# Kernel optimization log

Measured on AMD Instinct MI355X. Metric: run time of the kernel, lower is better.

The kernel has to match this reference:

```python
import jax, jax.numpy as jnp
import numpy as np

N = 100000
E = 1600000
IN_FEATS = 128
H_FEATS = 128
NUM_CLASSES = 64
BN_EPS = 1e-5


def setup_inputs() -> dict:
    key = jax.random.key(0)
    ks = jax.random.split(key, 16)
    inp = {
        "in_feat": jax.random.normal(ks[0], (N, IN_FEATS), dtype=jnp.float32),
        "src": jax.random.randint(ks[1], (E,), 0, N, dtype=jnp.int64),
        "dst": jax.random.randint(ks[2], (E,), 0, N, dtype=jnp.int64),
        # GraphConv weights (glorot-ish scale) and biases
        "W0": jax.random.normal(ks[3], (IN_FEATS, H_FEATS), dtype=jnp.float32) / np.sqrt(IN_FEATS),
        "b0": jnp.zeros((H_FEATS,), dtype=jnp.float32),
        "W1": jax.random.normal(ks[4], (H_FEATS, H_FEATS), dtype=jnp.float32) / np.sqrt(H_FEATS),
        "b1": jnp.zeros((H_FEATS,), dtype=jnp.float32),
        "W2": jax.random.normal(ks[5], (H_FEATS, NUM_CLASSES), dtype=jnp.float32) / np.sqrt(H_FEATS),
        "b2": jnp.zeros((NUM_CLASSES,), dtype=jnp.float32),
        # BatchNorm affine params
        "gamma0": jnp.ones((H_FEATS,), dtype=jnp.float32),
        "beta0": jnp.zeros((H_FEATS,), dtype=jnp.float32),
        "gamma1": jnp.ones((H_FEATS,), dtype=jnp.float32),
        "beta1": jnp.zeros((H_FEATS,), dtype=jnp.float32),
    }
    return inp


def _graph_conv(src, dst, h, W, b):
    # DGL GraphConv, norm='both': D_dst^{-1/2} A (D_src^{-1/2} h W) + b
    ones = jnp.ones((src.shape[0],), dtype=h.dtype)
    deg_out = jnp.clip(jax.ops.segment_sum(ones, src, num_segments=N), 1.0)
    deg_in = jnp.clip(jax.ops.segment_sum(ones, dst, num_segments=N), 1.0)
    h = h * jax.lax.rsqrt(deg_out)[:, None]
    h = h @ W  # mult weight before aggregation (same math either way)
    agg = jax.ops.segment_sum(h[src], dst, num_segments=N)  # SpMM
    return agg * jax.lax.rsqrt(deg_in)[:, None] + b


def _batch_norm(h, gamma, beta):
    # BatchNorm1d in training mode: biased batch stats over the node axis
    mean = jnp.mean(h, axis=0)
    var = jnp.mean(jnp.square(h - mean), axis=0)
    return (h - mean) * jax.lax.rsqrt(var + BN_EPS) * gamma + beta


def reference(in_feat, src, dst, W0, b0, W1, b1, W2, b2, gamma0, beta0, gamma1, beta1):
    h = _graph_conv(src, dst, in_feat, W0, b0)
    h = jax.nn.relu(_batch_norm(h, gamma0, beta0))  # dropout p=0 -> identity
    h = _graph_conv(src, dst, h, W1, b1)
    h = jax.nn.relu(_batch_norm(h, gamma1, beta1))
    return _graph_conv(src, dst, h, W2, b2)
```

## Files before the change

kernel.cpp:

```cpp
#include <hip/hip_runtime.h>

#define NFEAT 128
#define BT 2048
#define BSH 9
#define BSZ 512

static inline size_t align_up(size_t x, size_t a) { return (x + a - 1) & ~(a - 1); }

__device__ inline unsigned short f2bf(float f) {
  unsigned u = __float_as_uint(f);
  u += 0x7FFF + ((u >> 16) & 1);
  return (unsigned short)(u >> 16);
}

__global__ __launch_bounds__(256) void k_bcount(const int* __restrict__ src,
                                                const int* __restrict__ dst,
                                                int* __restrict__ cnt, int E, int nb, int NBK) {
  __shared__ int hD[256], hS[256];
  const int t = threadIdx.x, b = blockIdx.x;
  hD[t] = 0; hS[t] = 0;
  __syncthreads();
  const int e0 = b * BT, e1 = min(E, e0 + BT);
  for (int e = e0 + t; e < e1; e += 256) {
    atomicAdd(&hD[dst[e] >> BSH], 1);
    atomicAdd(&hS[src[e] >> BSH], 1);
  }
  __syncthreads();
  if (t < NBK) {
    cnt[t * nb + b] = hD[t];
    cnt[(NBK + t) * nb + b] = hS[t];
  }
}

__global__ __launch_bounds__(512) void k_scanA(const int* __restrict__ in,
                                               int* __restrict__ out,
                                               int* __restrict__ bsum, int n) {
  __shared__ int tmp[512];
  const int t = threadIdx.x;
  const int i = blockIdx.x * 512 + t;
  int v = (i < n) ? in[i] : 0;
  tmp[t] = v;
  __syncthreads();
  for (int off = 1; off < 512; off <<= 1) {
    int y = (t >= off) ? tmp[t - off] : 0;
    __syncthreads();
    tmp[t] += y;
    __syncthreads();
  }
  int incl = tmp[t];
  if (i < n) out[i] = incl - v;
  if (t == 511) bsum[blockIdx.x] = incl;
}

__global__ __launch_bounds__(1024) void k_scanB(const int* __restrict__ bsum,
                                                int* __restrict__ bscan, int nb1) {
  __shared__ int tmp[1024];
  const int t = threadIdx.x;
  int v = (t < nb1) ? bsum[t] : 0;
  tmp[t] = v;
  __syncthreads();
  for (int off = 1; off < 1024; off <<= 1) {
    int y = (t >= off) ? tmp[t - off] : 0;
    __syncthreads();
    tmp[t] += y;
    __syncthreads();
  }
  bscan[t] = tmp[t] - v;
}

__global__ __launch_bounds__(512) void k_scanC(int* __restrict__ out,
                                               const int* __restrict__ bscan, int n) {
  const int i = blockIdx.x * 512 + threadIdx.x;
  if (i < n) out[i] += bscan[blockIdx.x];
}

__global__ __launch_bounds__(256) void k_bplace(const int* __restrict__ src,
                                                const int* __restrict__ dst,
                                                const int* __restrict__ off,
                                                int* __restrict__ buf, int E, int nb, int NBK) {
  __shared__ int cD[256], cS[256];
  const int t = threadIdx.x, b = blockIdx.x;
  if (t < NBK) {
    cD[t] = off[t * nb + b];
    cS[t] = off[(NBK + t) * nb + b];
  }
  __syncthreads();
  const int e0 = b * BT, e1 = min(E, e0 + BT);
  for (int e = e0 + t; e < e1; e += 256) {
    int s = src[e];
    int d = dst[e];
    int pD = atomicAdd(&cD[d >> BSH], 1);
    buf[pD] = ((d & (BSZ - 1)) << 17) | s;
    int pS = atomicAdd(&cS[s >> BSH], 1);
    buf[pS] = s;
  }
}

__global__ __launch_bounds__(256) void k_bcsr(const int* __restrict__ buf,
                                              const int* __restrict__ off,
                                              int* __restrict__ row_ptr,
                                              float* __restrict__ rsq_in,
                                              int* __restrict__ col,
                                              int E, int nb, int NBK, int N) {
  const int k = blockIdx.x, t = threadIdx.x;
  const int lo = off[k * nb];
  const int hi = (k + 1 < NBK) ? off[(k + 1) * nb] : E;
  __shared__ int cnt[BSZ];
  __shared__ int sc[BSZ];
  __shared__ int part[64];
  cnt[t] = 0; cnt[t + 256] = 0;
  __syncthreads();
  for (int e = lo + t; e < hi; e += 256) atomicAdd(&cnt[((unsigned)buf[e]) >> 17], 1);
  __syncthreads();
  if (t < 64) {
    int r = 0;
#pragma unroll
    for (int j = 0; j < 8; ++j) r += cnt[t * 8 + j];
    part[t] = r;
  }
  __syncthreads();
  if (t == 0) {
    int run = 0;
    for (int i = 0; i < 64; ++i) { int v = part[i]; part[i] = run; run += v; }
  }
  __syncthreads();
  if (t < 64) {
    int run = part[t];
#pragma unroll
    for (int j = 0; j < 8; ++j) { int v = cnt[t * 8 + j]; sc[t * 8 + j] = run; run += v; }
  }
  __syncthreads();
  for (int idx = t; idx < BSZ; idx += 256) {
    int n = (k << BSH) + idx;
    if (n < N) {
      row_ptr[n] = lo + sc[idx];
      int c = cnt[idx]; if (c < 1) c = 1;
      rsq_in[n] = 1.0f / sqrtf((float)c);
    }
    cnt[idx] = sc[idx];
  }
  if (k == NBK - 1 && t == 0) row_ptr[N] = E;
  __syncthreads();
  for (int e = lo + t; e < hi; e += 256) {
    int w = buf[e];
    int p = atomicAdd(&cnt[((unsigned)w) >> 17], 1);
    col[lo + p] = w & 0x1FFFF;
  }
}

__global__ __launch_bounds__(256) void k_bdeg(const int* __restrict__ buf,
                                              const int* __restrict__ off,
                                              float* __restrict__ rsq_out,
                                              int E, int nb, int NBK, int N) {
  const int k = blockIdx.x, t = threadIdx.x;
  const int lo = off[(NBK + k) * nb];
  const int hi = (k + 1 < NBK) ? off[(NBK + k + 1) * nb] : 2 * E;
  __shared__ int cnt[BSZ];
  cnt[t] = 0; cnt[t + 256] = 0;
  __syncthreads();
  for (int e = lo + t; e < hi; e += 256) atomicAdd(&cnt[buf[e] & (BSZ - 1)], 1);
  __syncthreads();
  for (int idx = t; idx < BSZ; idx += 256) {
    int n = (k << BSH) + idx;
    if (n < N) {
      int c = cnt[idx]; if (c < 1) c = 1;
      rsq_out[n] = 1.0f / sqrtf((float)c);
    }
  }
}

#define GB_ROWS 64
#define GB_COLS 64
#define GK 16
#define XLD 68

__global__ __launch_bounds__(256) void k_gemm(
    const float* __restrict__ X, const float* __restrict__ W,
    unsigned short* __restrict__ Ybf, const float* __restrict__ rsq_out,
    const float* __restrict__ bnscale, const float* __restrict__ bnshift,
    int Nrows, int Ccols, int mode) {
  __shared__ __align__(16) float Xs[GK][XLD];
  __shared__ __align__(16) float Ws[GK][XLD];
  const int tid = threadIdx.x;
  const int tx = tid & 15;
  const int ty = tid >> 4;
  const int rowBase = blockIdx.x * GB_ROWS;
  const int colBase = blockIdx.y * GB_COLS;
  float acc[4][4] = {};

  for (int k0 = 0; k0 < NFEAT; k0 += GK) {
#pragma unroll
    for (int i = 0; i < 4; ++i) {
      int e = tid + i * 256;
      int r = e >> 4, k = e & 15;
      int gr = rowBase + r;
      float v = 0.0f;
      if (gr < Nrows) v = X[(size_t)gr * NFEAT + k0 + k];
      if (mode) {
        v = v * bnscale[k0 + k] + bnshift[k0 + k];
        v = v > 0.0f ? v : 0.0f;
      }
      Xs[k][r] = v;
    }
#pragma unroll
    for (int i = 0; i < 4; ++i) {
      int e = tid + i * 256;
      int k = e >> 6, c = e & 63;
      Ws[k][c] = W[(size_t)(k0 + k) * Ccols + colBase + c];
    }
    __syncthreads();
#pragma unroll
    for (int k = 0; k < GK; ++k) {
      const float4 xv = *(const float4*)&Xs[k][ty * 4];
      const float4 wv = *(const float4*)&Ws[k][tx * 4];
      acc[0][0] += xv.x * wv.x; acc[0][1] += xv.x * wv.y; acc[0][2] += xv.x * wv.z; acc[0][3] += xv.x * wv.w;
      acc[1][0] += xv.y * wv.x; acc[1][1] += xv.y * wv.y; acc[1][2] += xv.y * wv.z; acc[1][3] += xv.y * wv.w;
      acc[2][0] += xv.z * wv.x; acc[2][1] += xv.z * wv.y; acc[2][2] += xv.z * wv.z; acc[2][3] += xv.z * wv.w;
      acc[3][0] += xv.w * wv.x; acc[3][1] += xv.w * wv.y; acc[3][2] += xv.w * wv.z; acc[3][3] += xv.w * wv.w;
    }
    __syncthreads();
  }
#pragma unroll
  for (int i = 0; i < 4; ++i) {
    int gr = rowBase + ty * 4 + i;
    if (gr < Nrows) {
      float s = rsq_out[gr];
      ushort4 o;
      o.x = f2bf(acc[i][0] * s);
      o.y = f2bf(acc[i][1] * s);
      o.z = f2bf(acc[i][2] * s);
      o.w = f2bf(acc[i][3] * s);
      *(ushort4*)&Ybf[(size_t)gr * Ccols + colBase + tx * 4] = o;
    }
  }
}

template <int F>
__global__ __launch_bounds__(256) void k_spmm_bf(const int* __restrict__ row_ptr,
                                                 const int* __restrict__ colidx,
                                                 const unsigned short* __restrict__ xW,
                                                 float* __restrict__ out,
                                                 const float* __restrict__ rsq_in,
                                                 const float* __restrict__ bias, int Nrows) {
  constexpr int L = F / 8;
  const int node = blockIdx.x * (256 / L) + threadIdx.x / L;
  const int lane = threadIdx.x % L;
  if (node >= Nrows) return;
  const int e0 = row_ptr[node];
  const int e1 = row_ptr[node + 1];
  float acc[8] = {};
  int e = e0;
  for (; e + 1 < e1; e += 2) {
    int s0 = colidx[e];
    int s1 = colidx[e + 1];
    uint4 v0 = *(const uint4*)&xW[(size_t)s0 * F + lane * 8];
    uint4 v1 = *(const uint4*)&xW[(size_t)s1 * F + lane * 8];
    acc[0] += __uint_as_float(v0.x << 16); acc[1] += __uint_as_float(v0.x & 0xFFFF0000u);
    acc[2] += __uint_as_float(v0.y << 16); acc[3] += __uint_as_float(v0.y & 0xFFFF0000u);
    acc[4] += __uint_as_float(v0.z << 16); acc[5] += __uint_as_float(v0.z & 0xFFFF0000u);
    acc[6] += __uint_as_float(v0.w << 16); acc[7] += __uint_as_float(v0.w & 0xFFFF0000u);
    acc[0] += __uint_as_float(v1.x << 16); acc[1] += __uint_as_float(v1.x & 0xFFFF0000u);
    acc[2] += __uint_as_float(v1.y << 16); acc[3] += __uint_as_float(v1.y & 0xFFFF0000u);
    acc[4] += __uint_as_float(v1.z << 16); acc[5] += __uint_as_float(v1.z & 0xFFFF0000u);
    acc[6] += __uint_as_float(v1.w << 16); acc[7] += __uint_as_float(v1.w & 0xFFFF0000u);
  }
  if (e < e1) {
    int s0 = colidx[e];
    uint4 v0 = *(const uint4*)&xW[(size_t)s0 * F + lane * 8];
    acc[0] += __uint_as_float(v0.x << 16); acc[1] += __uint_as_float(v0.x & 0xFFFF0000u);
    acc[2] += __uint_as_float(v0.y << 16); acc[3] += __uint_as_float(v0.y & 0xFFFF0000u);
    acc[4] += __uint_as_float(v0.z << 16); acc[5] += __uint_as_float(v0.z & 0xFFFF0000u);
    acc[6] += __uint_as_float(v0.w << 16); acc[7] += __uint_as_float(v0.w & 0xFFFF0000u);
  }
  const float sc = rsq_in[node];
  float4 oA, oB;
  const float4 bA = *(const float4*)&bias[lane * 8];
  const float4 bB = *(const float4*)&bias[lane * 8 + 4];
  oA.x = acc[0] * sc + bA.x; oA.y = acc[1] * sc + bA.y;
  oA.z = acc[2] * sc + bA.z; oA.w = acc[3] * sc + bA.w;
  oB.x = acc[4] * sc + bB.x; oB.y = acc[5] * sc + bB.y;
  oB.z = acc[6] * sc + bB.z; oB.w = acc[7] * sc + bB.w;
  *(float4*)&out[(size_t)node * F + lane * 8] = oA;
  *(float4*)&out[(size_t)node * F + lane * 8 + 4] = oB;
}

__global__ __launch_bounds__(256) void k_bn_stats(const float* __restrict__ h,
                                                  float* __restrict__ sum,
                                                  float* __restrict__ sumsq, int Nrows) {
  const int f = threadIdx.x & 127;
  const int half = threadIdx.x >> 7;
  float s = 0.f, ss = 0.f;
  for (int r = blockIdx.x * 2 + half; r < Nrows; r += gridDim.x * 2) {
    float v = h[(size_t)r * NFEAT + f];
    s += v;
    ss += v * v;
  }
  __shared__ float ls[256], lss[256];
  ls[threadIdx.x] = s;
  lss[threadIdx.x] = ss;
  __syncthreads();
  if (half == 0) {
    atomicAdd(&sum[f], ls[f] + ls[f + 128]);
    atomicAdd(&sumsq[f], lss[f] + lss[f + 128]);
  }
}

__global__ __launch_bounds__(128) void k_bn_final(const float* __restrict__ sum,
                                                  const float* __restrict__ sumsq,
                                                  const float* __restrict__ gamma,
                                                  const float* __restrict__ beta,
                                                  float* __restrict__ scale,
                                                  float* __restrict__ shift, int Nrows) {
  int f = threadIdx.x;
  float inv_n = 1.0f / (float)Nrows;
  float mean = sum[f] * inv_n;
  float var = sumsq[f] * inv_n - mean * mean;
  if (var < 0.f) var = 0.f;
  float sc = gamma[f] * (1.0f / sqrtf(var + 1e-5f));
  scale[f] = sc;
  shift[f] = beta[f] - mean * sc;
}

extern "C" void kernel_launch(void* const* d_in, const int* in_sizes, int n_in,
                              void* d_out, int out_size, void* d_ws, size_t ws_size,
                              hipStream_t stream) {
  const float* in_feat = (const float*)d_in[0];
  const int* src = (const int*)d_in[1];
  const int* dst = (const int*)d_in[2];
  const float* W0 = (const float*)d_in[3];
  const float* b0 = (const float*)d_in[4];
  const float* W1 = (const float*)d_in[5];
  const float* b1 = (const float*)d_in[6];
  const float* W2 = (const float*)d_in[7];
  const float* b2 = (const float*)d_in[8];
  const float* gamma0 = (const float*)d_in[9];
  const float* beta0 = (const float*)d_in[10];
  const float* gamma1 = (const float*)d_in[11];
  const float* beta1 = (const float*)d_in[12];
  float* out = (float*)d_out;

  const int N = in_sizes[0] / NFEAT;
  const int E = in_sizes[1];
  const int C2 = in_sizes[7] / NFEAT;

  const int nb = (E + BT - 1) / BT;
  const int NBK = (N + BSZ - 1) / BSZ;
  const int L = 2 * NBK * nb;
  const int nb1 = (L + 511) / 512;

  char* p = (char*)d_ws;
  auto carve = [&](size_t bytes) {
    char* q = p;
    p += align_up(bytes, 256);
    return q;
  };
  int* cnt = (int*)carve((size_t)L * 4);
  int* off = (int*)carve((size_t)L * 4);
  int* bsum = (int*)carve(1024 * 4);
  int* bscan = (int*)carve(1024 * 4);
  int* row_ptr = (int*)carve((size_t)(N + 1) * 4);
  int* col = (int*)carve((size_t)E * 4);
  float* rsq_out = (float*)carve((size_t)N * 4);
  float* rsq_in = (float*)carve((size_t)N * 4);
  float* bn_sum0 = (float*)carve(128 * 4);
  float* bn_sumsq0 = (float*)carve(128 * 4);
  float* bn_sum1 = (float*)carve(128 * 4);
  float* bn_sumsq1 = (float*)carve(128 * 4);
  float* bn_scale0 = (float*)carve(128 * 4);
  float* bn_shift0 = (float*)carve(128 * 4);
  float* bn_scale1 = (float*)carve(128 * 4);
  float* bn_shift1 = (float*)carve(128 * 4);
  unsigned short* xWbf = (unsigned short*)carve((size_t)N * NFEAT * 2);
  float* bufB = (float*)carve((size_t)N * NFEAT * 4);
  int* buf = (int*)carve((size_t)2 * E * 4);

  hipMemsetAsync(bn_sum0, 0, 4 * 128 * 4, stream);

  k_bcount<<<nb, 256, 0, stream>>>(src, dst, cnt, E, nb, NBK);
  k_scanA<<<nb1, 512, 0, stream>>>(cnt, off, bsum, L);
  k_scanB<<<1, 1024, 0, stream>>>(bsum, bscan, nb1);
  k_scanC<<<nb1, 512, 0, stream>>>(off, bscan, L);
  k_bplace<<<nb, 256, 0, stream>>>(src, dst, off, buf, E, nb, NBK);
  k_bcsr<<<NBK, 256, 0, stream>>>(buf, off, row_ptr, rsq_in, col, E, nb, NBK, N);
  k_bdeg<<<NBK, 256, 0, stream>>>(buf, off, rsq_out, E, nb, NBK, N);

  const int GR = (N + GB_ROWS - 1) / GB_ROWS;

  k_gemm<<<dim3(GR, NFEAT / GB_COLS), 256, 0, stream>>>(in_feat, W0, xWbf, rsq_out,
                                                        nullptr, nullptr, N, NFEAT, 0);
  k_spmm_bf<NFEAT><<<(N + 15) / 16, 256, 0, stream>>>(row_ptr, col, xWbf, bufB, rsq_in, b0, N);
  k_bn_stats<<<512, 256, 0, stream>>>(bufB, bn_sum0, bn_sumsq0, N);
  k_bn_final<<<1, 128, 0, stream>>>(bn_sum0, bn_sumsq0, gamma0, beta0, bn_scale0, bn_shift0, N);

  k_gemm<<<dim3(GR, NFEAT / GB_COLS), 256, 0, stream>>>(bufB, W1, xWbf, rsq_out,
                                                        bn_scale0, bn_shift0, N, NFEAT, 1);
  k_spmm_bf<NFEAT><<<(N + 15) / 16, 256, 0, stream>>>(row_ptr, col, xWbf, bufB, rsq_in, b1, N);
  k_bn_stats<<<512, 256, 0, stream>>>(bufB, bn_sum1, bn_sumsq1, N);
  k_bn_final<<<1, 128, 0, stream>>>(bn_sum1, bn_sumsq1, gamma1, beta1, bn_scale1, bn_shift1, N);

  k_gemm<<<dim3(GR, 1), 256, 0, stream>>>(bufB, W2, xWbf, rsq_out,
                                          bn_scale1, bn_shift1, N, C2, 1);
  k_spmm_bf<64><<<(N + 31) / 32, 256, 0, stream>>>(row_ptr, col, xWbf, out, rsq_in, b2, N);
}
```

Baseline: 571.9 us.

## Replace FP32 SIMT GEMM with bf16 MFMA GEMM using swizzled LDS

Replaces the scalar FP32 tiled GEMM with a matrix-core kernel that uses the 16x16x32 bf16 MFMA. Weights are pre-transposed and converted to bf16 by a new prep kernel. Each block loads a 64-row slab of activations once, converting it to bf16 with the BN+ReLU fused in, and computes every output column into XOR-swizzled LDS, so the old two-column-block grid that reread X twice goes away. The cost being removed is ALU-bound FP32 FMA throughput and the duplicated loads of X. In exchange the GEMM inputs are rounded to bf16, and the output stores are scalar 2-byte writes.

Result: faster. 516.5 us (-9.7%).

```diff
diff --git a/kernel.cpp b/kernel.cpp
--- a/kernel.cpp
+++ b/kernel.cpp
@@ -4,6 +4,9 @@
 #define BT 2048
 #define BSH 9
 #define BSZ 512
+
+typedef __attribute__((ext_vector_type(8))) short short8v;
+typedef __attribute__((ext_vector_type(4))) float float4v;
 
 static inline size_t align_up(size_t x, size_t a) { return (x + a - 1) & ~(a - 1); }
 
@@ -169,68 +172,105 @@
   }
 }
 
-#define GB_ROWS 64
-#define GB_COLS 64
-#define GK 16
-#define XLD 68
-
-__global__ __launch_bounds__(256) void k_gemm(
-    const float* __restrict__ X, const float* __restrict__ W,
+__global__ __launch_bounds__(256) void k_wprep(const float* __restrict__ W0,
+                                               const float* __restrict__ W1,
+                                               const float* __restrict__ W2,
+                                               unsigned short* __restrict__ Wt0,
+                                               unsigned short* __restrict__ Wt1,
+                                               unsigned short* __restrict__ Wt2) {
+  int t = blockIdx.x * 256 + threadIdx.x;
+  if (t < 16384) {
+    int c = t >> 7, k = t & 127;
+    Wt0[c * 128 + k] = f2bf(W0[k * 128 + c]);
+  } else if (t < 32768) {
+    int u = t - 16384;
+    int c = u >> 7, k = u & 127;
+    Wt1[c * 128 + k] = f2bf(W1[k * 128 + c]);
+  } else if (t < 40960) {
+    int u = t - 32768;
+    int c = u >> 7, k = u & 127;
+    Wt2[c * 128 + k] = f2bf(W2[k * 64 + c]);
+  }
+}
+
+template <int CC>
+__global__ __launch_bounds__(256) void k_gemm_mfma(
+    const float* __restrict__ X, const unsigned short* __restrict__ Wt,
     unsigned short* __restrict__ Ybf, const float* __restrict__ rsq_out,
     const float* __restrict__ bnscale, const float* __restrict__ bnshift,
-    int Nrows, int Ccols, int mode) {
-  __shared__ __align__(16) float Xs[GK][XLD];
-  __shared__ __align__(16) float Ws[GK][XLD];
+    int Nrows, int mode) {
+  constexpr int XBYTES = 64 * 256;
+  constexpr int WBYTES = CC * 256;
+  __shared__ __align__(16) char lds[XBYTES + WBYTES];
   const int tid = threadIdx.x;
-  const int tx = tid & 15;
-  const int ty = tid >> 4;
-  const int rowBase = blockIdx.x * GB_ROWS;
-  const int colBase = blockIdx.y * GB_COLS;
-  float acc[4][4] = {};
-
-  for (int k0 = 0; k0 < NFEAT; k0 += GK) {
-#pragma unroll
-    for (int i = 0; i < 4; ++i) {
-      int e = tid + i * 256;
-      int r = e >> 4, k = e & 15;
-      int gr = rowBase + r;
-      float v = 0.0f;
-      if (gr < Nrows) v = X[(size_t)gr * NFEAT + k0 + k];
-      if (mode) {
-        v = v * bnscale[k0 + k] + bnshift[k0 + k];
-        v = v > 0.0f ? v : 0.0f;
-      }
-      Xs[k][r] = v;
+  const int rowBase = blockIdx.x * 64;
+
+  for (int u = tid; u < CC * 16; u += 256) {
+    int c = u >> 4, kq = u & 15;
+    uint4 v = *(const uint4*)(Wt + c * 128 + kq * 8);
+    int byte = (c * 256 + kq * 16) ^ ((c & 7) << 4);
+    *(uint4*)(&lds[XBYTES + byte]) = v;
+  }
+#pragma unroll
+  for (int i = 0; i < 8; ++i) {
+    int u = tid + i * 256;
+    int r = u >> 5, kq = u & 31;
+    int gr = rowBase + r;
+    float4 v = make_float4(0.f, 0.f, 0.f, 0.f);
+    if (gr < Nrows) v = *(const float4*)(X + (size_t)gr * 128 + kq * 4);
+    if (mode) {
+      const float4 s = *(const float4*)(bnscale + kq * 4);
+      const float4 h = *(const float4*)(bnshift + kq * 4);
+      v.x = fmaxf(v.x * s.x + h.x, 0.f);
+      v.y = fmaxf(v.y * s.y + h.y, 0.f);
+      v.z = fmaxf(v.z * s.z + h.z, 0.f);
+      v.w = fmaxf(v.w * s.w + h.w, 0.f);
     }
-#pragma unroll
-    for (int i = 0; i < 4; ++i) {
-      int e = tid + i * 256;
-      int k = e >> 6, c = e & 63;
-      Ws[k][c] = W[(size_t)(k0 + k) * Ccols + colBase + c];
+    ushort4 o;
+    o.x = f2bf(v.x); o.y = f2bf(v.y); o.z = f2bf(v.z); o.w = f2bf(v.w);
+    int byte = (r * 256 + kq * 8) ^ ((r & 7) << 4);
+    *(ushort4*)(&lds[byte]) = o;
+  }
+  __syncthreads();
+
+  const int wv = tid >> 6;
+  const int l = tid & 63;
+  const int l16 = l & 15, lk = l >> 4;
+
+  short8v a[4];
+  const int arow = wv * 16 + l16;
+#pragma unroll
+  for (int kk = 0; kk < 4; ++kk) {
+    int byte = (arow * 256 + kk * 64 + lk * 16) ^ ((arow & 7) << 4);
+    a[kk] = *(const short8v*)(&lds[byte]);
+  }
+
+  float4v acc[CC / 16];
+#pragma unroll
+  for (int ct = 0; ct < CC / 16; ++ct) acc[ct] = (float4v){0.f, 0.f, 0.f, 0.f};
+
+#pragma unroll
+  for (int ct = 0; ct < CC / 16; ++ct) {
+    const int col = ct * 16 + l16;
+#pragma unroll
+    for (int kk = 0; kk < 4; ++kk) {
+      int byte = XBYTES + ((col * 256 + kk * 64 + lk * 16) ^ ((col & 7) << 4));
+      short8v b = *(const short8v*)(&lds[byte]);
+      acc[ct] = __builtin_amdgcn_mfma_f32_16x16x32_bf16(a[kk], b, acc[ct], 0, 0, 0);
     }
-    __syncthreads();
-#pragma unroll
-    for (int k = 0; k < GK; ++k) {
-      const float4 xv = *(const float4*)&Xs[k][ty * 4];
-      const float4 wv = *(const float4*)&Ws[k][tx * 4];
-      acc[0][0] += xv.x * wv.x; acc[0][1] += xv.x * wv.y; acc[0][2] += xv.x * wv.z; acc[0][3] += xv.x * wv.w;
-      acc[1][0] += xv.y * wv.x; acc[1][1] += xv.y * wv.y; acc[1][2] += xv.y * wv.z; acc[1][3] += xv.y * wv.w;
-      acc[2][0] += xv.z * wv.x; acc[2][1] += xv.z * wv.y; acc[2][2] += xv.z * wv.z; acc[2][3] += xv.z * wv.w;
-      acc[3][0] += xv.w * wv.x; acc[3][1] += xv.w * wv.y; acc[3][2] += xv.w * wv.z; acc[3][3] += xv.w * wv.w;
-    }
-    __syncthreads();
-  }
-#pragma unroll
-  for (int i = 0; i < 4; ++i) {
-    int gr = rowBase + ty * 4 + i;
-    if (gr < Nrows) {
-      float s = rsq_out[gr];
-      ushort4 o;
-      o.x = f2bf(acc[i][0] * s);
-      o.y = f2bf(acc[i][1] * s);
-      o.z = f2bf(acc[i][2] * s);
-      o.w = f2bf(acc[i][3] * s);
-      *(ushort4*)&Ybf[(size_t)gr * Ccols + colBase + tx * 4] = o;
+  }
+
+  const int row0 = rowBase + wv * 16 + lk * 4;
+  float scr[4];
+#pragma unroll
+  for (int r = 0; r < 4; ++r) scr[r] = (row0 + r < Nrows) ? rsq_out[row0 + r] : 0.f;
+#pragma unroll
+  for (int ct = 0; ct < CC / 16; ++ct) {
+#pragma unroll
+    for (int r = 0; r < 4; ++r) {
+      int row = row0 + r;
+      if (row < Nrows)
+        Ybf[(size_t)row * CC + ct * 16 + l16] = f2bf(acc[ct][r] * scr[r]);
     }
   }
 }
@@ -341,7 +381,6 @@
 
   const int N = in_sizes[0] / NFEAT;
   const int E = in_sizes[1];
-  const int C2 = in_sizes[7] / NFEAT;
 
   const int nb = (E + BT - 1) / BT;
   const int NBK = (N + BSZ - 1) / BSZ;
@@ -370,12 +409,16 @@
   float* bn_shift0 = (float*)carve(128 * 4);
   float* bn_scale1 = (float*)carve(128 * 4);
   float* bn_shift1 = (float*)carve(128 * 4);
+  unsigned short* Wt0 = (unsigned short*)carve(16384 * 2);
+  unsigned short* Wt1 = (unsigned short*)carve(16384 * 2);
+  unsigned short* Wt2 = (unsigned short*)carve(8192 * 2);
   unsigned short* xWbf = (unsigned short*)carve((size_t)N * NFEAT * 2);
   float* bufB = (float*)carve((size_t)N * NFEAT * 4);
   int* buf = (int*)carve((size_t)2 * E * 4);
 
   hipMemsetAsync(bn_sum0, 0, 4 * 128 * 4, stream);
 
+  k_wprep<<<160, 256, 0, stream>>>(W0, W1, W2, Wt0, Wt1, Wt2);
   k_bcount<<<nb, 256, 0, stream>>>(src, dst, cnt, E, nb, NBK);
   k_scanA<<<nb1, 512, 0, stream>>>(cnt, off, bsum, L);
   k_scanB<<<1, 1024, 0, stream>>>(bsum, bscan, nb1);
@@ -384,21 +427,21 @@
   k_bcsr<<<NBK, 256, 0, stream>>>(buf, off, row_ptr, rsq_in, col, E, nb, NBK, N);
   k_bdeg<<<NBK, 256, 0, stream>>>(buf, off, rsq_out, E, nb, NBK, N);
 
-  const int GR = (N + GB_ROWS - 1) / GB_ROWS;
-
-  k_gemm<<<dim3(GR, NFEAT / GB_COLS), 256, 0, stream>>>(in_feat, W0, xWbf, rsq_out,
-                                                        nullptr, nullptr, N, NFEAT, 0);
+  const int GR = (N + 63) / 64;
+
+  k_gemm_mfma<128><<<GR, 256, 0, stream>>>(in_feat, Wt0, xWbf, rsq_out,
+                                           nullptr, nullptr, N, 0);
   k_spmm_bf<NFEAT><<<(N + 15) / 16, 256, 0, stream>>>(row_ptr, col, xWbf, bufB, rsq_in, b0, N);
   k_bn_stats<<<512, 256, 0, stream>>>(bufB, bn_sum0, bn_sumsq0, N);
   k_bn_final<<<1, 128, 0, stream>>>(bn_sum0, bn_sumsq0, gamma0, beta0, bn_scale0, bn_shift0, N);
 
-  k_gemm<<<dim3(GR, NFEAT / GB_COLS), 256, 0, stream>>>(bufB, W1, xWbf, rsq_out,
-                                                        bn_scale0, bn_shift0, N, NFEAT, 1);
+  k_gemm_mfma<128><<<GR, 256, 0, stream>>>(bufB, Wt1, xWbf, rsq_out,
+                                           bn_scale0, bn_shift0, N, 1);
   k_spmm_bf<NFEAT><<<(N + 15) / 16, 256, 0, stream>>>(row_ptr, col, xWbf, bufB, rsq_in, b1, N);
   k_bn_stats<<<512, 256, 0, stream>>>(bufB, bn_sum1, bn_sumsq1, N);
   k_bn_final<<<1, 128, 0, stream>>>(bn_sum1, bn_sumsq1, gamma1, beta1, bn_scale1, bn_shift1, N);
 
-  k_gemm<<<dim3(GR, 1), 256, 0, stream>>>(bufB, W2, xWbf, rsq_out,
-                                          bn_scale1, bn_shift1, N, C2, 1);
+  k_gemm_mfma<64><<<GR, 256, 0, stream>>>(bufB, Wt2, xWbf, rsq_out,
+                                          bn_scale1, bn_shift1, N, 1);
   k_spmm_bf<64><<<(N + 31) / 32, 256, 0, stream>>>(row_ptr, col, xWbf, out, rsq_in, b2, N);
 }
```
